# Optimization experiments

Measured on AMD Instinct MI355X. Metric: run time of the kernel, lower is better.

Reference implementation:

```python
import jax, jax.numpy as jnp
import numpy as np
from jax import lax

H = W = 8
N = H * W            # grid cells
D = 34               # token dim = 16 + 16 + 2
NH = 2               # attention heads
FF = 2048            # torch TransformerEncoderLayer default dim_feedforward
EPS = 1e-5


def setup_inputs():
    key = jax.random.key(0)
    ks = iter(jax.random.split(key, 64))
    rn = lambda shape, s=0.05: jax.random.normal(next(ks), shape, jnp.float32) * s
    inp = {"obs": jax.random.normal(next(ks), (2, H, W), jnp.float32), "action": 2}
    inp["conv1_w"] = rn((16, 2, 3, 3)); inp["conv1_b"] = rn((16,))
    inp["conv2_w"] = rn((16, 16, 3, 3)); inp["conv2_b"] = rn((16,))
    for l in range(2):
        p = f"l{l}_"
        inp[p + "in_w"] = rn((3 * D, D)); inp[p + "in_b"] = rn((3 * D,))
        inp[p + "out_w"] = rn((D, D)); inp[p + "out_b"] = rn((D,))
        inp[p + "ff1_w"] = rn((FF, D)); inp[p + "ff1_b"] = rn((FF,))
        inp[p + "ff2_w"] = rn((D, FF)); inp[p + "ff2_b"] = rn((D,))
        inp[p + "ln1_g"] = jnp.ones((D,)); inp[p + "ln1_b"] = jnp.zeros((D,))
        inp[p + "ln2_g"] = jnp.ones((D,)); inp[p + "ln2_b"] = jnp.zeros((D,))
    inp["act_w"] = rn((8, 4)); inp["act_b"] = rn((8,))
    inp["head_w"] = rn((16, D + 8)); inp["head_b"] = rn((16,))
    return inp


def _ln(x, g, b):
    m = x.mean(-1, keepdims=True)
    v = ((x - m) ** 2).mean(-1, keepdims=True)
    return (x - m) * lax.rsqrt(v + EPS) * g + b


def _mha(x, in_w, in_b, out_w, out_b):
    S = x.shape[0]
    hd = D // NH
    qkv = x @ in_w.T + in_b                          # [S, 3D]
    q, k, v = jnp.split(qkv, 3, axis=-1)
    q = q.reshape(S, NH, hd).transpose(1, 0, 2)      # [H, S, hd]
    k = k.reshape(S, NH, hd).transpose(1, 0, 2)
    v = v.reshape(S, NH, hd).transpose(1, 0, 2)
    attn = jax.nn.softmax(jnp.einsum('hsd,htd->hst', q, k) * (1.0 / float(np.sqrt(hd))), axis=-1)
    o = jnp.einsum('hst,htd->hsd', attn, v).transpose(1, 0, 2).reshape(S, D)
    return o @ out_w.T + out_b


def _layer(x, in_w, in_b, out_w, out_b, ff1_w, ff1_b, ff2_w, ff2_b, ln1_g, ln1_b, ln2_g, ln2_b):
    # torch default post-norm, relu activation, dropout off (eval)
    x = _ln(x + _mha(x, in_w, in_b, out_w, out_b), ln1_g, ln1_b)
    h = jax.nn.relu(x @ ff1_w.T + ff1_b) @ ff2_w.T + ff2_b
    return _ln(x + h, ln2_g, ln2_b)


def _forward(obs, conv1_w, conv1_b, conv2_w, conv2_b, layers, act_w, act_b, head_w, head_b, action):
    x = obs[None]                                    # [1, 2, H, W]
    dn = ('NCHW', 'OIHW', 'NCHW')
    x = jax.nn.relu(lax.conv_general_dilated(x, conv1_w, (1, 1), 'SAME', dimension_numbers=dn) + conv1_b[None, :, None, None])
    x = jax.nn.relu(lax.conv_general_dilated(x, conv2_w, (1, 1), 'SAME', dimension_numbers=dn) + conv2_b[None, :, None, None])
    cell = x.reshape(16, N).T                        # [N, 16]
    # vectorized pairwise relation tokens (replaces O(N^2) python loop)
    r = (jnp.arange(N) // W).astype(jnp.float32)
    c = (jnp.arange(N) % W).astype(jnp.float32)
    dx = (r[:, None] - r[None, :]) / ((H - 1) / 2.0)
    dy = (c[:, None] - c[None, :]) / ((W - 1) / 2.0)
    rel = jnp.stack([dx, dy], axis=-1)               # [N, N, 2]
    a = jnp.broadcast_to(cell[:, None, :], (N, N, 16))
    b = jnp.broadcast_to(cell[None, :, :], (N, N, 16))
    seq = jnp.concatenate([a, b, rel], axis=-1).reshape(N * N, D)
    for p in layers:
        seq = _layer(seq, *p)
    agent_idx = jnp.argmax(obs[0].reshape(-1))
    agent_tok = lax.dynamic_slice_in_dim(seq, agent_idx * N, N, 0)  # rows for agent cell
    hvec = agent_tok.mean(0)
    a_emb = jax.nn.relu(jax.nn.one_hot(action, 4, dtype=jnp.float32) @ act_w.T + act_b)
    return (jnp.concatenate([hvec, a_emb]) @ head_w.T + head_b)[None]


def reference(obs, action, conv1_w, conv1_b, conv2_w, conv2_b,
              l0_in_w, l0_in_b, l0_out_w, l0_out_b, l0_ff1_w, l0_ff1_b, l0_ff2_w, l0_ff2_b,
              l0_ln1_g, l0_ln1_b, l0_ln2_g, l0_ln2_b,
              l1_in_w, l1_in_b, l1_out_w, l1_out_b, l1_ff1_w, l1_ff1_b, l1_ff2_w, l1_ff2_b,
              l1_ln1_g, l1_ln1_b, l1_ln2_g, l1_ln2_b,
              act_w, act_b, head_w, head_b):
    layers = [
        (l0_in_w, l0_in_b, l0_out_w, l0_out_b, l0_ff1_w, l0_ff1_b, l0_ff2_w, l0_ff2_b, l0_ln1_g, l0_ln1_b, l0_ln2_g, l0_ln2_b),
        (l1_in_w, l1_in_b, l1_out_w, l1_out_b, l1_ff1_w, l1_ff1_b, l1_ff2_w, l1_ff2_b, l1_ln1_g, l1_ln1_b, l1_ln2_g, l1_ln2_b),
    ]
    return _forward(obs, conv1_w, conv1_b, conv2_w, conv2_b, layers, act_w, act_b, head_w, head_b, action)
```

## Files before the change

### kernel.cpp

```cpp
#include <hip/hip_runtime.h>
#include <math.h>

#define SEQ 4096
#define DIM 34
#define NHEAD 2
#define HD 17
#define FFDIM 2048
#define SC2 0.34990494f

#define EXP2F(x) __builtin_amdgcn_exp2f(x)
#define MFMA16(a, b, c) __builtin_amdgcn_mfma_f32_16x16x32_bf16(a, b, c, 0, 0, 0)

typedef unsigned short u16;
typedef __attribute__((ext_vector_type(8))) short bf16x8;
typedef __attribute__((ext_vector_type(4))) float f32x4;

__device__ inline u16 f2bf(float f) {
    uint32_t u = __builtin_bit_cast(uint32_t, f);
    u += 0x7fffu + ((u >> 16) & 1u);
    return (u16)(u >> 16);
}
__device__ inline uint32_t pack2(float a, float b) {
    uint32_t ua = __builtin_bit_cast(uint32_t, a);
    ua += 0x7fffu + ((ua >> 16) & 1u);
    uint32_t ub = __builtin_bit_cast(uint32_t, b);
    ub += 0x7fffu + ((ub >> 16) & 1u);
    return (ua >> 16) | (ub & 0xffff0000u);
}

#define W1B_ELEMS (FFDIM * 64)
#define W2B_ELEMS (48 * FFDIM)
#define NWCONV 448
#define NQT (SEQ / 16)

__global__ __launch_bounds__(1024) void wm_pre(
    const float* __restrict__ obs,
    const float* __restrict__ c1w, const float* __restrict__ c1b,
    const float* __restrict__ c2w, const float* __restrict__ c2b,
    const float* __restrict__ in_w, const float* __restrict__ in_b,
    float* __restrict__ x, u16* __restrict__ Qb, u16* __restrict__ Kb,
    u16* __restrict__ Vc, u16* __restrict__ V16)
{
    const int tid = threadIdx.x;
    __shared__ float obsp[2][10][10];
    __shared__ float h1p[16][10][10];
    __shared__ float cs[64][17];
    const int sb = blockIdx.x;
    const int t0 = sb * 64;

    for (int e = tid; e < 200; e += 1024) ((float*)obsp)[e] = 0.f;
    for (int e = tid; e < 1600; e += 1024) ((float*)h1p)[e] = 0.f;
    __syncthreads();
    if (tid < 128) {
        int i = tid >> 6, n = tid & 63, y = n >> 3, xx = n & 7;
        obsp[i][y + 1][xx + 1] = obs[tid];
    }
    __syncthreads();
    {
        int o = tid >> 6, n = tid & 63, y = n >> 3, xx = n & 7;
        float a = c1b[o];
        #pragma unroll
        for (int i = 0; i < 2; ++i)
            #pragma unroll
            for (int ky = 0; ky < 3; ++ky)
                #pragma unroll
                for (int kx = 0; kx < 3; ++kx)
                    a = fmaf(obsp[i][y + ky][xx + kx], c1w[((o*2 + i)*3 + ky)*3 + kx], a);
        h1p[o][y + 1][xx + 1] = fmaxf(a, 0.f);
    }
    __syncthreads();
    {
        int o = tid >> 6, n = tid & 63, y = n >> 3, xx = n & 7;
        float a = c2b[o];
        #pragma unroll
        for (int i = 0; i < 16; ++i)
            #pragma unroll
            for (int ky = 0; ky < 3; ++ky)
                #pragma unroll
                for (int kx = 0; kx < 3; ++kx)
                    a = fmaf(h1p[i][y + ky][xx + kx], c2w[((o*16 + i)*3 + ky)*3 + kx], a);
        cs[n][o] = fmaxf(a, 0.f);
    }
    __syncthreads();
    for (int e = tid; e < 64 * DIM; e += 1024) {
        int tl = e / DIM, d = e % DIM;
        int t = t0 + tl, i = t >> 6, j = t & 63;
        float v;
        if (d < 16)       v = cs[i][d];
        else if (d < 32)  v = cs[j][d - 16];
        else if (d == 32) v = (float)((i >> 3) - (j >> 3)) * (1.0f / 3.5f);
        else              v = (float)((i & 7) - (j & 7)) * (1.0f / 3.5f);
        x[t0 * DIM + e] = v;
    }
    for (int ii = 0; ii < 11; ++ii) {
        int e = tid + ii * 1024;
        if (e >= 64 * 162) break;
        int t = t0 + (e & 63), slot = e >> 6;
        int i = t >> 6, j = t & 63;
        float dx = (float)((i >> 3) - (j >> 3)) * (1.0f / 3.5f);
        float dy = (float)((i & 7) - (j & 7)) * (1.0f / 3.5f);
        if (slot < 128) {
            int isK = slot >> 6, h2 = (slot >> 5) & 1, hs = slot & 31;
            float val = 0.f;
            if (hs < HD) {
                int row = isK*DIM + h2*HD + hs;
                const float* wr = in_w + row*DIM;
                float a = in_b[row];
                #pragma unroll
                for (int d = 0; d < 16; ++d) a = fmaf(cs[i][d], wr[d], a);
                #pragma unroll
                for (int d = 0; d < 16; ++d) a = fmaf(cs[j][d], wr[16 + d], a);
                a = fmaf(dx, wr[32], a);
                a = fmaf(dy, wr[33], a);
                val = isK ? a : a * SC2;
            } else if (hs == HD) {
                val = isK ? 1.0f : -8.0f;
            }
            u16* dst = isK ? Kb : Qb;
            dst[(((size_t)h2*SEQ + t) << 5) + hs] = f2bf(val);
        } else {
            int s = slot - 128;
            int h2 = s >= HD, dd = s - h2*HD;
            int row = 2*DIM + h2*HD + dd;
            const float* wr = in_w + row*DIM;
            float a = in_b[row];
            #pragma unroll
            for (int d = 0; d < 16; ++d) a = fmaf(cs[i][d], wr[d], a);
            #pragma unroll
            for (int d = 0; d < 16; ++d) a = fmaf(cs[j][d], wr[16 + d], a);
            a = fmaf(dx, wr[32], a);
            a = fmaf(dy, wr[33], a);
            u16 v = f2bf(a);
            if (dd == 16) V16[h2*SEQ + t] = v;
            else {
                int c = t >> 5, g = (t >> 3) & 3, ix = t & 7;
                Vc[((((size_t)h2*128 + c)*4 + g)*16 + dd)*8 + ix] = v;
            }
        }
    }
}

__global__ __launch_bounds__(1024) void wm_attn3(const u16* __restrict__ Qb,
        const u16* __restrict__ Kb, const u16* __restrict__ Vc,
        const u16* __restrict__ V16, float* __restrict__ x,
        const float* __restrict__ ow, const float* __restrict__ obias,
        const float* __restrict__ g, const float* __restrict__ be,
        const float* __restrict__ w1a, const float* __restrict__ b1a, const float* __restrict__ w2a,
        const float* __restrict__ w1b, const float* __restrict__ b1b, const float* __restrict__ w2b,
        u16* __restrict__ W1A, u16* __restrict__ W2A,
        u16* __restrict__ W1B, u16* __restrict__ W2B)
{
    const int qt = blockIdx.x;
    const int tid = threadIdx.x;
    if (qt >= NQT) {
        int id = (qt - NQT) * 1024 + tid;
        const int half = W1B_ELEMS + W2B_ELEMS;
        const float* w1 = w1a; const float* b1 = b1a; const float* w2 = w2a;
        u16* W1 = W1A; u16* W2 = W2A;
        if (id >= half) { id -= half; w1 = w1b; b1 = b1b; w2 = w2b; W1 = W1B; W2 = W2B; }
        if (id < W1B_ELEMS) {
            int n = id >> 6, c = id & 63;
            float v = (c < DIM) ? w1[n*DIM + c] : ((c == DIM) ? b1[n] : 0.f);
            W1[id] = f2bf(v);
        } else {
            int e = id - W1B_ELEMS;
            int n = e >> 11;
            float v = (n < DIM) ? w2[(n << 11) + (e & 2047)] : 0.f;
            W2[e] = f2bf(v);
        }
        return;
    }
    const int wv = tid >> 6, l = tid & 63;
    const int h = wv >> 3, rr = wv & 7;
    const int q = l & 15, gg = l >> 4;

    __shared__ float red[16][64][7];
    __shared__ float os[16][DIM];
    __shared__ float ys[16][DIM];
    __shared__ float stats[16][2];

    const u16* Qh = Qb + (((size_t)h*SEQ + qt*16 + q) << 5) + 8*gg;
    const u16* Kh = Kb + ((size_t)h*SEQ << 5);
    const u16* Vh = Vc + (size_t)h*128*512;
    const u16* V6 = V16 + (size_t)h*SEQ;

    const bf16x8 qf = *(const bf16x8*)Qh;
    const f32x4 zero4 = {0.f, 0.f, 0.f, 0.f};
    bf16x8 onesv;
    { union { uint32_t u[4]; bf16x8 v; } o1;
      o1.u[0] = o1.u[1] = o1.u[2] = o1.u[3] = 0x3F803F80u; onesv = o1.v; }

    f32x4 olo = zero4, ohi = zero4;
    const int srcA = q + 32*(gg & 1);
    const int srcB = srcA + 16;
    const bool hi = (gg >= 2);

    for (int it = 0; it < 8; ++it) {
        const int cA = rr*16 + it*2;
        const int k0 = cA * 32;
        bf16x8 kf0 = *(const bf16x8*)(Kh + ((size_t)(k0 + q) << 5) + 8*gg);
        bf16x8 kf1 = *(const bf16x8*)(Kh + ((size_t)(k0 + 16 + q) << 5) + 8*gg);
        bf16x8 kf2 = *(const bf16x8*)(Kh + ((size_t)(k0 + 32 + q) << 5) + 8*gg);
        bf16x8 kf3 = *(const bf16x8*)(Kh + ((size_t)(k0 + 48 + q) << 5) + 8*gg);
        f32x4 s0 = MFMA16(kf0, qf, zero4);
        f32x4 s1 = MFMA16(kf1, qf, zero4);
        f32x4 s2 = MFMA16(kf2, qf, zero4);
        f32x4 s3 = MFMA16(kf3, qf, zero4);
        float pa0 = EXP2F(s0[0]), pa1 = EXP2F(s0[1]), pa2 = EXP2F(s0[2]), pa3 = EXP2F(s0[3]);
        float pa4 = EXP2F(s1[0]), pa5 = EXP2F(s1[1]), pa6 = EXP2F(s1[2]), pa7 = EXP2F(s1[3]);
        float pb0 = EXP2F(s2[0]), pb1 = EXP2F(s2[1]), pb2 = EXP2F(s2[2]), pb3 = EXP2F(s2[3]);
        float pb4 = EXP2F(s3[0]), pb5 = EXP2F(s3[1]), pb6 = EXP2F(s3[2]), pb7 = EXP2F(s3[3]);
        {
            uint32_t a0t0 = pack2(pa0, pa1), a1t0 = pack2(pa2, pa3);
            uint32_t a0t1 = pack2(pa4, pa5), a1t1 = pack2(pa6, pa7);
            uint32_t w0a = (uint32_t)__shfl((int)a0t0, srcA), w0b = (uint32_t)__shfl((int)a0t1, srcA);
            uint32_t w1a_ = (uint32_t)__shfl((int)a1t0, srcA), w1b_ = (uint32_t)__shfl((int)a1t1, srcA);
            uint32_t w2a_ = (uint32_t)__shfl((int)a0t0, srcB), w2b_ = (uint32_t)__shfl((int)a0t1, srcB);
            uint32_t w3a = (uint32_t)__shfl((int)a1t0, srcB), w3b = (uint32_t)__shfl((int)a1t1, srcB);
            union { uint32_t u[4]; bf16x8 v; } pu;
            pu.u[0] = hi ? w0b : w0a;
            pu.u[1] = hi ? w1b_ : w1a_;
            pu.u[2] = hi ? w2b_ : w2a_;
            pu.u[3] = hi ? w3b : w3a;
            bf16x8 vf = *(const bf16x8*)(Vh + (size_t)(cA*4 + gg)*128 + q*8);
            bf16x8 v6 = {};
            if (q == 0) v6 = *(const bf16x8*)(V6 + k0 + 8*gg);
            else if (q == 1) v6 = onesv;
            olo = MFMA16(vf, pu.v, olo);
            ohi = MFMA16(v6, pu.v, ohi);
        }
        {
            uint32_t a0t0 = pack2(pb0, pb1), a1t0 = pack2(pb2, pb3);
            uint32_t a0t1 = pack2(pb4, pb5), a1t1 = pack2(pb6, pb7);
            uint32_t w0a = (uint32_t)__shfl((int)a0t0, srcA), w0b = (uint32_t)__shfl((int)a0t1, srcA);
            uint32_t w1a_ = (uint32_t)__shfl((int)a1t0, srcA), w1b_ = (uint32_t)__shfl((int)a1t1, srcA);
            uint32_t w2a_ = (uint32_t)__shfl((int)a0t0, srcB), w2b_ = (uint32_t)__shfl((int)a0t1, srcB);
            uint32_t w3a = (uint32_t)__shfl((int)a1t0, srcB), w3b = (uint32_t)__shfl((int)a1t1, srcB);
            union { uint32_t u[4]; bf16x8 v; } pu;
            pu.u[0] = hi ? w0b : w0a;
            pu.u[1] = hi ? w1b_ : w1a_;
            pu.u[2] = hi ? w2b_ : w2a_;
            pu.u[3] = hi ? w3b : w3a;
            bf16x8 vf = *(const bf16x8*)(Vh + (size_t)((cA + 1)*4 + gg)*128 + q*8);
            bf16x8 v6 = {};
            if (q == 0) v6 = *(const bf16x8*)(V6 + k0 + 32 + 8*gg);
            else if (q == 1) v6 = onesv;
            olo = MFMA16(vf, pu.v, olo);
            ohi = MFMA16(v6, pu.v, ohi);
        }
    }

    {
        float* r = red[wv][l];
        r[0] = ohi[1];
        r[1] = olo[0]; r[2] = olo[1]; r[3] = olo[2]; r[4] = olo[3];
        r[5] = ohi[0];
    }
    __syncthreads();
    if (rr == 0) {
        float lt = 0.f, o0 = 0.f, o1 = 0.f, o2 = 0.f, o3 = 0.f, o6 = 0.f;
        #pragma unroll
        for (int p = 0; p < 8; ++p) {
            float* r = red[wv + p][l];
            lt += r[0]; o0 += r[1]; o1 += r[2]; o2 += r[3]; o3 += r[4]; o6 += r[5];
        }
        lt += __shfl_xor(lt, 16);
        lt += __shfl_xor(lt, 32);
        float inv = 1.f / lt;
        os[q][h*HD + 4*gg + 0] = o0*inv;
        os[q][h*HD + 4*gg + 1] = o1*inv;
        os[q][h*HD + 4*gg + 2] = o2*inv;
        os[q][h*HD + 4*gg + 3] = o3*inv;
        if (gg == 0) os[q][h*HD + 16] = o6*inv;
    }
    __syncthreads();
    for (int e = tid; e < 16 * DIM; e += 1024) {
        int tt = e / DIM, d = e % DIM;
        const float* wr = ow + d*DIM;
        float acc = obias[d];
        #pragma unroll
        for (int k = 0; k < DIM; ++k) acc = fmaf(os[tt][k], wr[k], acc);
        ys[tt][d] = x[(size_t)(qt*16 + tt)*DIM + d] + acc;
    }
    __syncthreads();
    if (tid < 16) {
        float s1 = 0.f, s2 = 0.f;
        #pragma unroll
        for (int d = 0; d < DIM; ++d) { float v = ys[tid][d]; s1 += v; s2 += v*v; }
        float mean = s1 * (1.0f / DIM);
        float var  = s2 * (1.0f / DIM) - mean*mean;
        stats[tid][0] = mean;
        stats[tid][1] = rsqrtf(var + 1e-5f);
    }
    __syncthreads();
    for (int e = tid; e < 16 * DIM; e += 1024) {
        int tt = e / DIM, d = e % DIM;
        x[(size_t)(qt*16 + tt)*DIM + d] = (ys[tt][d] - stats[tt][0]) * stats[tt][1] * g[d] + be[d];
    }
}

__global__ __launch_bounds__(1024) void wm_ff3(float* __restrict__ x,
        const u16* __restrict__ W1b, const u16* __restrict__ W2b,
        const float* __restrict__ b2, const float* __restrict__ g,
        const float* __restrict__ be,
        const float* __restrict__ in_w, const float* __restrict__ in_b,
        u16* __restrict__ Qb, u16* __restrict__ Kb,
        u16* __restrict__ Vc, u16* __restrict__ V16, int do_qkv)
{
    __shared__ u16 Hs[16][16][128];
    __shared__ float red[16][16][52];
    __shared__ float ys[16][DIM];
    __shared__ float stats[16][2];
    const int tid = threadIdx.x, wv = tid >> 6, l = tid & 63;
    const int q = l & 15, g4 = l >> 4;
    const int t0 = blockIdx.x * 16;

    const float* xr = x + (size_t)(t0 + q) * DIM;
    union { uint32_t u[4]; bf16x8 v; } a0, a1;
    #pragma unroll
    for (int j = 0; j < 4; ++j)
        a0.u[j] = pack2(xr[g4*8 + 2*j], xr[g4*8 + 2*j + 1]);
    a1.u[0] = 0; a1.u[1] = 0; a1.u[2] = 0; a1.u[3] = 0;
    if (g4 == 0) {
        a1.u[0] = pack2(xr[32], xr[33]);
        a1.u[1] = pack2(1.0f, 0.f);
    }
    const f32x4 zero4 = {0.f, 0.f, 0.f, 0.f};

    const int hbase = wv * 128;
    #pragma unroll
    for (int nt = 0; nt < 8; ++nt) {
        const u16* brow = W1b + (size_t)(hbase + nt*16 + q) * 64 + g4*8;
        bf16x8 b0 = *(const bf16x8*)brow;
        bf16x8 b1f = *(const bf16x8*)(brow + 32);
        f32x4 c = MFMA16(a0.v, b0, zero4);
        c = MFMA16(a1.v, b1f, c);
        #pragma unroll
        for (int r = 0; r < 4; ++r) {
            int mm = 4*g4 + r;
            int byte = ((nt*16 + q) * 2) ^ ((mm & 7) << 4);
            *(u16*)((char*)&Hs[wv][mm][0] + byte) = f2bf(fmaxf(c[r], 0.f));
        }
    }
    asm volatile("s_waitcnt lgkmcnt(0)" ::: "memory");
    __builtin_amdgcn_sched_barrier(0);
    f32x4 acc0 = zero4, acc1 = zero4, acc2 = zero4;
    #pragma unroll
    for (int ks = 0; ks < 4; ++ks) {
        int byte = (ks*64 + g4*16) ^ ((q & 7) << 4);
        bf16x8 af = *(const bf16x8*)((char*)&Hs[wv][q][0] + byte);
        const u16* bp = W2b + (size_t)q * FFDIM + hbase + ks*32 + g4*8;
        acc0 = MFMA16(af, *(const bf16x8*)bp, acc0);
        acc1 = MFMA16(af, *(const bf16x8*)(bp + 16*FFDIM), acc1);
        acc2 = MFMA16(af, *(const bf16x8*)(bp + 32*FFDIM), acc2);
    }
    #pragma unroll
    for (int r = 0; r < 4; ++r) {
        red[wv][4*g4 + r][q]      = acc0[r];
        red[wv][4*g4 + r][16 + q] = acc1[r];
        red[wv][4*g4 + r][32 + q] = acc2[r];
    }
    __syncthreads();
    for (int e = tid; e < 16*DIM; e += 1024) {
        int tt = e / DIM, d = e % DIM;
        float v = x[(size_t)(t0 + tt)*DIM + d] + b2[d];
        #pragma unroll
        for (int w = 0; w < 16; ++w) v += red[w][tt][d];
        ys[tt][d] = v;
    }
    __syncthreads();
    if (tid < 16) {
        float s1 = 0.f, s2 = 0.f;
        #pragma unroll
        for (int d = 0; d < DIM; ++d) { float v = ys[tid][d]; s1 += v; s2 += v * v; }
        float mean = s1 * (1.0f / DIM);
        float var  = s2 * (1.0f / DIM) - mean * mean;
        stats[tid][0] = mean;
        stats[tid][1] = rsqrtf(var + 1e-5f);
    }
    __syncthreads();
    for (int e = tid; e < 16*DIM; e += 1024) {
        int tt = e / DIM, d = e % DIM;
        float v = (ys[tt][d] - stats[tt][0]) * stats[tt][1] * g[d] + be[d];
        x[(size_t)(t0 + tt)*DIM + d] = v;
        ys[tt][d] = v;
    }
    if (do_qkv) {
        __syncthreads();
        #pragma unroll
        for (int ii = 0; ii < 2; ++ii) {
            int e = tid + ii*1024;
            if (e < 16*102) {
                int r = e >> 4, tt = e & 15;
                const float* wr = in_w + r*DIM;
                float a = in_b[r];
                #pragma unroll
                for (int d = 0; d < DIM; ++d) a = fmaf(ys[tt][d], wr[d], a);
                int tg = t0 + tt;
                if (r < 68) {
                    int rq = (r < 34) ? r : r - 34;
                    int h2 = rq >= HD, hs = rq - h2*HD;
                    u16 v = f2bf((r < 34) ? a*SC2 : a);
                    u16* dst = (r < 34) ? Qb : Kb;
                    dst[(((size_t)h2*SEQ + tg) << 5) + hs] = v;
                } else {
                    int rv = r - 68;
                    int h2 = rv >= HD, dd = rv - h2*HD;
                    u16 v = f2bf(a);
                    if (dd == 16) V16[h2*SEQ + tg] = v;
                    else {
                        int c = tg >> 5, gg = (tg >> 3) & 3, ix = tg & 7;
                        Vc[((((size_t)h2*128 + c)*4 + gg)*16 + dd)*8 + ix] = v;
                    }
                }
            }
        }
    }
}

__global__ __launch_bounds__(64) void wm_final(const float* __restrict__ x,
        const float* __restrict__ obs, const int* __restrict__ action,
        const float* __restrict__ aw, const float* __restrict__ ab,
        const float* __restrict__ hw, const float* __restrict__ hb,
        float* __restrict__ out)
{
    __shared__ float hv[DIM];
    __shared__ float saemb[8];
    __shared__ int sai;
    const int tid = threadIdx.x;
    {
        float v = obs[tid];
        float mx = v;
        for (int off = 32; off; off >>= 1) mx = fmaxf(mx, __shfl_xor(mx, off));
        unsigned long long mask = __ballot(v == mx);
        if (tid == 0) sai = (int)(__ffsll(mask) - 1);
    }
    if (tid < 8) {
        int act = *action;
        saemb[tid] = fmaxf(aw[tid*4 + act] + ab[tid], 0.f);
    }
    __syncthreads();
    const int ai = sai;
    if (tid < DIM) {
        float s = 0.f;
        for (int r = 0; r < 64; ++r) s += x[(size_t)(ai*64 + r)*DIM + tid];
        hv[tid] = s * (1.0f / 64.0f);
    }
    __syncthreads();
    if (tid < 16) {
        float a = hb[tid];
        #pragma unroll
        for (int d = 0; d < DIM; ++d) a = fmaf(hv[d], hw[tid*42 + d], a);
        #pragma unroll
        for (int j = 0; j < 8; ++j) a = fmaf(saemb[j], hw[tid*42 + DIM + j], a);
        out[tid] = a;
    }
}

extern "C" void kernel_launch(void* const* d_in, const int* in_sizes, int n_in,
                              void* d_out, int out_size, void* d_ws, size_t ws_size,
                              hipStream_t stream)
{
    const float* obs    = (const float*)d_in[0];
    const int*   action = (const int*)  d_in[1];

    float* ws   = (float*)d_ws;
    float* x    = ws + 1056;
    float* o    = x + SEQ * DIM;
    u16*   Qb   = (u16*)(o + SEQ * DIM);
    u16*   Kb   = Qb + 2 * SEQ * 32;
    u16*   Vc   = Kb + 2 * SEQ * 32;
    u16*   V16  = Vc + 2 * 128 * 512;
    u16*   W1b0 = V16 + 2 * SEQ;
    u16*   W2b0 = W1b0 + W1B_ELEMS;
    u16*   W1b1 = W2b0 + W2B_ELEMS;
    u16*   W2b1 = W1b1 + W1B_ELEMS;

    wm_pre<<<64, 1024, 0, stream>>>(
        obs, (const float*)d_in[2], (const float*)d_in[3],
        (const float*)d_in[4], (const float*)d_in[5],
        (const float*)d_in[6], (const float*)d_in[7],
        x, Qb, Kb, Vc, V16);

    wm_attn3<<<NQT + NWCONV, 1024, 0, stream>>>(Qb, Kb, Vc, V16, x,
        (const float*)d_in[8], (const float*)d_in[9],
        (const float*)d_in[14], (const float*)d_in[15],
        (const float*)d_in[10], (const float*)d_in[11], (const float*)d_in[12],
        (const float*)d_in[22], (const float*)d_in[23], (const float*)d_in[24],
        W1b0, W2b0, W1b1, W2b1);

    wm_ff3<<<NQT, 1024, 0, stream>>>(x, W1b0, W2b0,
        (const float*)d_in[13], (const float*)d_in[16], (const float*)d_in[17],
        (const float*)d_in[18], (const float*)d_in[19],
        Qb, Kb, Vc, V16, 1);

    wm_attn3<<<NQT, 1024, 0, stream>>>(Qb, Kb, Vc, V16, x,
        (const float*)d_in[20], (const float*)d_in[21],
        (const float*)d_in[26], (const float*)d_in[27],
        (const float*)d_in[10], (const float*)d_in[11], (const float*)d_in[12],
        (const float*)d_in[22], (const float*)d_in[23], (const float*)d_in[24],
        W1b0, W2b0, W1b1, W2b1);

    wm_ff3<<<NQT, 1024, 0, stream>>>(x, W1b1, W2b1,
        (const float*)d_in[25], (const float*)d_in[28], (const float*)d_in[29],
        (const float*)d_in[18], (const float*)d_in[19],
        Qb, Kb, Vc, V16, 0);

    wm_final<<<1, 64, 0, stream>>>(x, obs, action,
        (const float*)d_in[30], (const float*)d_in[31],
        (const float*)d_in[32], (const float*)d_in[33], (float*)d_out);
}
```

Before: 95.93 us.

## Split attention keys across two blocks and fuse out-proj/LN1 into FF kernel

Each query tile's attention is now split into two blocks, each covering half the keys. Each block writes unnormalized partial outputs and softmax denominators to a workspace buffer. The FF kernel combines the two partials, normalizes, and then applies the output projection and LN1 before the feed-forward step. This doubles attention-grid parallelism and removes the serial epilogue from the attention kernel, at the cost of extra global traffic for the partials and more work in the FF kernel.

After: 96.16 us. Within noise of the previous version (+0.2%).

```diff
diff --git a/kernel.cpp b/kernel.cpp
--- a/kernel.cpp
+++ b/kernel.cpp
@@ -32,6 +32,7 @@
 #define W2B_ELEMS (48 * FFDIM)
 #define NWCONV 448
 #define NQT (SEQ / 16)
+#define POS 36
 
 __global__ __launch_bounds__(1024) void wm_pre(
     const float* __restrict__ obs,
@@ -140,20 +141,18 @@
     }
 }
 
-__global__ __launch_bounds__(1024) void wm_attn3(const u16* __restrict__ Qb,
+__global__ __launch_bounds__(1024, 8) void wm_attn5(const u16* __restrict__ Qb,
         const u16* __restrict__ Kb, const u16* __restrict__ Vc,
-        const u16* __restrict__ V16, float* __restrict__ x,
-        const float* __restrict__ ow, const float* __restrict__ obias,
-        const float* __restrict__ g, const float* __restrict__ be,
+        const u16* __restrict__ V16, float* __restrict__ po,
         const float* __restrict__ w1a, const float* __restrict__ b1a, const float* __restrict__ w2a,
         const float* __restrict__ w1b, const float* __restrict__ b1b, const float* __restrict__ w2b,
         u16* __restrict__ W1A, u16* __restrict__ W2A,
         u16* __restrict__ W1B, u16* __restrict__ W2B)
 {
-    const int qt = blockIdx.x;
+    const int bid = blockIdx.x;
     const int tid = threadIdx.x;
-    if (qt >= NQT) {
-        int id = (qt - NQT) * 1024 + tid;
+    if (bid >= 2 * NQT) {
+        int id = (bid - 2 * NQT) * 1024 + tid;
         const int half = W1B_ELEMS + W2B_ELEMS;
         const float* w1 = w1a; const float* b1 = b1a; const float* w2 = w2a;
         u16* W1 = W1A; u16* W2 = W2A;
@@ -170,14 +169,12 @@
         }
         return;
     }
+    const int qt = bid >> 1, khalf = bid & 1;
     const int wv = tid >> 6, l = tid & 63;
     const int h = wv >> 3, rr = wv & 7;
     const int q = l & 15, gg = l >> 4;
 
     __shared__ float red[16][64][7];
-    __shared__ float os[16][DIM];
-    __shared__ float ys[16][DIM];
-    __shared__ float stats[16][2];
 
     const u16* Qh = Qb + (((size_t)h*SEQ + qt*16 + q) << 5) + 8*gg;
     const u16* Kh = Kb + ((size_t)h*SEQ << 5);
@@ -195,8 +192,8 @@
     const int srcB = srcA + 16;
     const bool hi = (gg >= 2);
 
-    for (int it = 0; it < 8; ++it) {
-        const int cA = rr*16 + it*2;
+    for (int it = 0; it < 4; ++it) {
+        const int cA = khalf*64 + rr*8 + it*2;
         const int k0 = cA * 32;
         bf16x8 kf0 = *(const bf16x8*)(Kh + ((size_t)(k0 + q) << 5) + 8*gg);
         bf16x8 kf1 = *(const bf16x8*)(Kh + ((size_t)(k0 + 16 + q) << 5) + 8*gg);
@@ -266,40 +263,19 @@
         }
         lt += __shfl_xor(lt, 16);
         lt += __shfl_xor(lt, 32);
-        float inv = 1.f / lt;
-        os[q][h*HD + 4*gg + 0] = o0*inv;
-        os[q][h*HD + 4*gg + 1] = o1*inv;
-        os[q][h*HD + 4*gg + 2] = o2*inv;
-        os[q][h*HD + 4*gg + 3] = o3*inv;
-        if (gg == 0) os[q][h*HD + 16] = o6*inv;
-    }
-    __syncthreads();
-    for (int e = tid; e < 16 * DIM; e += 1024) {
-        int tt = e / DIM, d = e % DIM;
-        const float* wr = ow + d*DIM;
-        float acc = obias[d];
-        #pragma unroll
-        for (int k = 0; k < DIM; ++k) acc = fmaf(os[tt][k], wr[k], acc);
-        ys[tt][d] = x[(size_t)(qt*16 + tt)*DIM + d] + acc;
-    }
-    __syncthreads();
-    if (tid < 16) {
-        float s1 = 0.f, s2 = 0.f;
-        #pragma unroll
-        for (int d = 0; d < DIM; ++d) { float v = ys[tid][d]; s1 += v; s2 += v*v; }
-        float mean = s1 * (1.0f / DIM);
-        float var  = s2 * (1.0f / DIM) - mean*mean;
-        stats[tid][0] = mean;
-        stats[tid][1] = rsqrtf(var + 1e-5f);
-    }
-    __syncthreads();
-    for (int e = tid; e < 16 * DIM; e += 1024) {
-        int tt = e / DIM, d = e % DIM;
-        x[(size_t)(qt*16 + tt)*DIM + d] = (ys[tt][d] - stats[tt][0]) * stats[tt][1] * g[d] + be[d];
+        float* prow = po + ((size_t)khalf*SEQ + qt*16 + q) * POS;
+        prow[h*HD + 4*gg + 0] = o0;
+        prow[h*HD + 4*gg + 1] = o1;
+        prow[h*HD + 4*gg + 2] = o2;
+        prow[h*HD + 4*gg + 3] = o3;
+        if (gg == 0) { prow[h*HD + 16] = o6; prow[34 + h] = lt; }
     }
 }
 
 __global__ __launch_bounds__(1024) void wm_ff3(float* __restrict__ x,
+        const float* __restrict__ po,
+        const float* __restrict__ ow, const float* __restrict__ obias,
+        const float* __restrict__ ln1g, const float* __restrict__ ln1b,
         const u16* __restrict__ W1b, const u16* __restrict__ W2b,
         const float* __restrict__ b2, const float* __restrict__ g,
         const float* __restrict__ be,
@@ -307,22 +283,60 @@
         u16* __restrict__ Qb, u16* __restrict__ Kb,
         u16* __restrict__ Vc, u16* __restrict__ V16, int do_qkv)
 {
-    __shared__ u16 Hs[16][16][128];
+    __shared__ union { u16 Hs[16][16][128]; float os[16][POS]; } sa;
     __shared__ float red[16][16][52];
     __shared__ float ys[16][DIM];
     __shared__ float stats[16][2];
+    __shared__ float xt[16][DIM + 2];
     const int tid = threadIdx.x, wv = tid >> 6, l = tid & 63;
     const int q = l & 15, g4 = l >> 4;
     const int t0 = blockIdx.x * 16;
 
-    const float* xr = x + (size_t)(t0 + q) * DIM;
+    for (int e = tid; e < 16 * POS; e += 1024) {
+        int tt = e / POS, c = e % POS;
+        sa.os[tt][c] = po[(size_t)(t0 + tt)*POS + c]
+                     + po[(size_t)(SEQ + t0 + tt)*POS + c];
+    }
+    __syncthreads();
+    if (tid < 32) stats[tid >> 1][tid & 1] = 1.f / sa.os[tid >> 1][34 + (tid & 1)];
+    __syncthreads();
+    for (int e = tid; e < 16 * DIM; e += 1024) {
+        int tt = e / DIM, d = e % DIM;
+        sa.os[tt][d] *= stats[tt][d >= HD];
+    }
+    __syncthreads();
+    for (int e = tid; e < 16 * DIM; e += 1024) {
+        int tt = e / DIM, d = e % DIM;
+        const float* wr = ow + d*DIM;
+        float acc = obias[d];
+        #pragma unroll
+        for (int k = 0; k < DIM; ++k) acc = fmaf(sa.os[tt][k], wr[k], acc);
+        ys[tt][d] = x[(size_t)(t0 + tt)*DIM + d] + acc;
+    }
+    __syncthreads();
+    if (tid < 16) {
+        float s1 = 0.f, s2 = 0.f;
+        #pragma unroll
+        for (int d = 0; d < DIM; ++d) { float v = ys[tid][d]; s1 += v; s2 += v*v; }
+        float mean = s1 * (1.0f / DIM);
+        float var  = s2 * (1.0f / DIM) - mean*mean;
+        stats[tid][0] = mean;
+        stats[tid][1] = rsqrtf(var + 1e-5f);
+    }
+    __syncthreads();
+    for (int e = tid; e < 16 * DIM; e += 1024) {
+        int tt = e / DIM, d = e % DIM;
+        xt[tt][d] = (ys[tt][d] - stats[tt][0]) * stats[tt][1] * ln1g[d] + ln1b[d];
+    }
+    __syncthreads();
+
     union { uint32_t u[4]; bf16x8 v; } a0, a1;
     #pragma unroll
     for (int j = 0; j < 4; ++j)
-        a0.u[j] = pack2(xr[g4*8 + 2*j], xr[g4*8 + 2*j + 1]);
+        a0.u[j] = pack2(xt[q][g4*8 + 2*j], xt[q][g4*8 + 2*j + 1]);
     a1.u[0] = 0; a1.u[1] = 0; a1.u[2] = 0; a1.u[3] = 0;
     if (g4 == 0) {
-        a1.u[0] = pack2(xr[32], xr[33]);
+        a1.u[0] = pack2(xt[q][32], xt[q][33]);
         a1.u[1] = pack2(1.0f, 0.f);
     }
     const f32x4 zero4 = {0.f, 0.f, 0.f, 0.f};
@@ -339,7 +353,7 @@
         for (int r = 0; r < 4; ++r) {
             int mm = 4*g4 + r;
             int byte = ((nt*16 + q) * 2) ^ ((mm & 7) << 4);
-            *(u16*)((char*)&Hs[wv][mm][0] + byte) = f2bf(fmaxf(c[r], 0.f));
+            *(u16*)((char*)&sa.Hs[wv][mm][0] + byte) = f2bf(fmaxf(c[r], 0.f));
         }
     }
     asm volatile("s_waitcnt lgkmcnt(0)" ::: "memory");
@@ -348,7 +362,7 @@
     #pragma unroll
     for (int ks = 0; ks < 4; ++ks) {
         int byte = (ks*64 + g4*16) ^ ((q & 7) << 4);
-        bf16x8 af = *(const bf16x8*)((char*)&Hs[wv][q][0] + byte);
+        bf16x8 af = *(const bf16x8*)((char*)&sa.Hs[wv][q][0] + byte);
         const u16* bp = W2b + (size_t)q * FFDIM + hbase + ks*32 + g4*8;
         acc0 = MFMA16(af, *(const bf16x8*)bp, acc0);
         acc1 = MFMA16(af, *(const bf16x8*)(bp + 16*FFDIM), acc1);
@@ -363,7 +377,7 @@
     __syncthreads();
     for (int e = tid; e < 16*DIM; e += 1024) {
         int tt = e / DIM, d = e % DIM;
-        float v = x[(size_t)(t0 + tt)*DIM + d] + b2[d];
+        float v = xt[tt][d] + b2[d];
         #pragma unroll
         for (int w = 0; w < 16; ++w) v += red[w][tt][d];
         ys[tt][d] = v;
@@ -475,6 +489,7 @@
     u16*   W2b0 = W1b0 + W1B_ELEMS;
     u16*   W1b1 = W2b0 + W2B_ELEMS;
     u16*   W2b1 = W1b1 + W1B_ELEMS;
+    float* po   = (float*)(W2b1 + W2B_ELEMS);
 
     wm_pre<<<64, 1024, 0, stream>>>(
         obs, (const float*)d_in[2], (const float*)d_in[3],
@@ -482,26 +497,28 @@
         (const float*)d_in[6], (const float*)d_in[7],
         x, Qb, Kb, Vc, V16);
 
-    wm_attn3<<<NQT + NWCONV, 1024, 0, stream>>>(Qb, Kb, Vc, V16, x,
-        (const float*)d_in[8], (const float*)d_in[9],
-        (const float*)d_in[14], (const float*)d_in[15],
+    wm_attn5<<<2*NQT + NWCONV, 1024, 0, stream>>>(Qb, Kb, Vc, V16, po,
         (const float*)d_in[10], (const float*)d_in[11], (const float*)d_in[12],
         (const float*)d_in[22], (const float*)d_in[23], (const float*)d_in[24],
         W1b0, W2b0, W1b1, W2b1);
 
-    wm_ff3<<<NQT, 1024, 0, stream>>>(x, W1b0, W2b0,
+    wm_ff3<<<NQT, 1024, 0, stream>>>(x, po,
+        (const float*)d_in[8], (const float*)d_in[9],
+        (const float*)d_in[14], (const float*)d_in[15],
+        W1b0, W2b0,
         (const float*)d_in[13], (const float*)d_in[16], (const float*)d_in[17],
         (const float*)d_in[18], (const float*)d_in[19],
         Qb, Kb, Vc, V16, 1);
 
-    wm_attn3<<<NQT, 1024, 0, stream>>>(Qb, Kb, Vc, V16, x,
-        (const float*)d_in[20], (const float*)d_in[21],
-        (const float*)d_in[26], (const float*)d_in[27],
+    wm_attn5<<<2*NQT, 1024, 0, stream>>>(Qb, Kb, Vc, V16, po,
         (const float*)d_in[10], (const float*)d_in[11], (const float*)d_in[12],
         (const float*)d_in[22], (const float*)d_in[23], (const float*)d_in[24],
         W1b0, W2b0, W1b1, W2b1);
 
-    wm_ff3<<<NQT, 1024, 0, stream>>>(x, W1b1, W2b1,
+    wm_ff3<<<NQT, 1024, 0, stream>>>(x, po,
+        (const float*)d_in[20], (const float*)d_in[21],
+        (const float*)d_in[26], (const float*)d_in[27],
+        W1b1, W2b1,
         (const float*)d_in[25], (const float*)d_in[28], (const float*)d_in[29],
         (const float*)d_in[18], (const float*)d_in[19],
         Qb, Kb, Vc, V16, 0);
```

## Halve rows per FF block and split prologue into more blocks

Applied to the files above, without the earlier changes.

The feed-forward kernel now handles 8 tokens per block instead of 16, launching twice as many blocks. MFMA tiles are still 16 rows, so half of each tile is zero-padded, and the LDS buffers and swizzle are resized to match. The pre kernel also spreads its token and QKV work over 256 blocks of 16 tokens instead of 64 blocks of 64. The aim is better CU occupancy and load spread across the GPU. The cost is MFMA work wasted on padded rows and the per-block weight reads (W1/W2) being repeated twice as often, and the pre kernel now recomputes the convolution in four times as many blocks.

Result: slower. 113.3 us (+18.1%).

```diff
diff --git a/kernel.cpp b/kernel.cpp
--- a/kernel.cpp
+++ b/kernel.cpp
@@ -45,8 +45,7 @@
     __shared__ float obsp[2][10][10];
     __shared__ float h1p[16][10][10];
     __shared__ float cs[64][17];
-    const int sb = blockIdx.x;
-    const int t0 = sb * 64;
+    const int t0 = blockIdx.x * 16;
 
     for (int e = tid; e < 200; e += 1024) ((float*)obsp)[e] = 0.f;
     for (int e = tid; e < 1600; e += 1024) ((float*)h1p)[e] = 0.f;
@@ -82,7 +81,7 @@
         cs[n][o] = fmaxf(a, 0.f);
     }
     __syncthreads();
-    for (int e = tid; e < 64 * DIM; e += 1024) {
+    for (int e = tid; e < 16 * DIM; e += 1024) {
         int tl = e / DIM, d = e % DIM;
         int t = t0 + tl, i = t >> 6, j = t & 63;
         float v;
@@ -90,12 +89,12 @@
         else if (d < 32)  v = cs[j][d - 16];
         else if (d == 32) v = (float)((i >> 3) - (j >> 3)) * (1.0f / 3.5f);
         else              v = (float)((i & 7) - (j & 7)) * (1.0f / 3.5f);
-        x[t0 * DIM + e] = v;
-    }
-    for (int ii = 0; ii < 11; ++ii) {
+        x[(size_t)t0 * DIM + e] = v;
+    }
+    for (int ii = 0; ii < 3; ++ii) {
         int e = tid + ii * 1024;
-        if (e >= 64 * 162) break;
-        int t = t0 + (e & 63), slot = e >> 6;
+        if (e >= 16 * 162) break;
+        int t = t0 + (e & 15), slot = e >> 4;
         int i = t >> 6, j = t & 63;
         float dx = (float)((i >> 3) - (j >> 3)) * (1.0f / 3.5f);
         float dy = (float)((i & 7) - (j & 7)) * (1.0f / 3.5f);
@@ -299,7 +298,7 @@
     }
 }
 
-__global__ __launch_bounds__(1024) void wm_ff3(float* __restrict__ x,
+__global__ __launch_bounds__(1024, 8) void wm_ff3(float* __restrict__ x,
         const u16* __restrict__ W1b, const u16* __restrict__ W2b,
         const float* __restrict__ b2, const float* __restrict__ g,
         const float* __restrict__ be,
@@ -307,23 +306,26 @@
         u16* __restrict__ Qb, u16* __restrict__ Kb,
         u16* __restrict__ Vc, u16* __restrict__ V16, int do_qkv)
 {
-    __shared__ u16 Hs[16][16][128];
-    __shared__ float red[16][16][52];
-    __shared__ float ys[16][DIM];
-    __shared__ float stats[16][2];
+    __shared__ u16 Hs[16][8][128];
+    __shared__ float red[16][8][52];
+    __shared__ float ys[8][DIM];
+    __shared__ float stats[8][2];
     const int tid = threadIdx.x, wv = tid >> 6, l = tid & 63;
     const int q = l & 15, g4 = l >> 4;
-    const int t0 = blockIdx.x * 16;
-
-    const float* xr = x + (size_t)(t0 + q) * DIM;
+    const int t0 = blockIdx.x * 8;
+
     union { uint32_t u[4]; bf16x8 v; } a0, a1;
-    #pragma unroll
-    for (int j = 0; j < 4; ++j)
-        a0.u[j] = pack2(xr[g4*8 + 2*j], xr[g4*8 + 2*j + 1]);
+    a0.u[0] = 0; a0.u[1] = 0; a0.u[2] = 0; a0.u[3] = 0;
     a1.u[0] = 0; a1.u[1] = 0; a1.u[2] = 0; a1.u[3] = 0;
-    if (g4 == 0) {
-        a1.u[0] = pack2(xr[32], xr[33]);
-        a1.u[1] = pack2(1.0f, 0.f);
+    if (q < 8) {
+        const float* xr = x + (size_t)(t0 + q) * DIM;
+        #pragma unroll
+        for (int j = 0; j < 4; ++j)
+            a0.u[j] = pack2(xr[g4*8 + 2*j], xr[g4*8 + 2*j + 1]);
+        if (g4 == 0) {
+            a1.u[0] = pack2(xr[32], xr[33]);
+            a1.u[1] = pack2(1.0f, 0.f);
+        }
     }
     const f32x4 zero4 = {0.f, 0.f, 0.f, 0.f};
 
@@ -335,11 +337,13 @@
         bf16x8 b1f = *(const bf16x8*)(brow + 32);
         f32x4 c = MFMA16(a0.v, b0, zero4);
         c = MFMA16(a1.v, b1f, c);
-        #pragma unroll
-        for (int r = 0; r < 4; ++r) {
-            int mm = 4*g4 + r;
-            int byte = ((nt*16 + q) * 2) ^ ((mm & 7) << 4);
-            *(u16*)((char*)&Hs[wv][mm][0] + byte) = f2bf(fmaxf(c[r], 0.f));
+        if (g4 < 2) {
+            #pragma unroll
+            for (int r = 0; r < 4; ++r) {
+                int mm = 4*g4 + r;
+                int byte = ((nt*16 + q) * 2) ^ (mm << 5);
+                *(u16*)((char*)&Hs[wv][mm][0] + byte) = f2bf(fmaxf(c[r], 0.f));
+            }
         }
     }
     asm volatile("s_waitcnt lgkmcnt(0)" ::: "memory");
@@ -347,21 +351,26 @@
     f32x4 acc0 = zero4, acc1 = zero4, acc2 = zero4;
     #pragma unroll
     for (int ks = 0; ks < 4; ++ks) {
-        int byte = (ks*64 + g4*16) ^ ((q & 7) << 4);
-        bf16x8 af = *(const bf16x8*)((char*)&Hs[wv][q][0] + byte);
+        bf16x8 af = {};
+        if (q < 8) {
+            int byte = (ks*64 + g4*16) ^ (q << 5);
+            af = *(const bf16x8*)((char*)&Hs[wv][q][0] + byte);
+        }
         const u16* bp = W2b + (size_t)q * FFDIM + hbase + ks*32 + g4*8;
         acc0 = MFMA16(af, *(const bf16x8*)bp, acc0);
         acc1 = MFMA16(af, *(const bf16x8*)(bp + 16*FFDIM), acc1);
         acc2 = MFMA16(af, *(const bf16x8*)(bp + 32*FFDIM), acc2);
     }
-    #pragma unroll
-    for (int r = 0; r < 4; ++r) {
-        red[wv][4*g4 + r][q]      = acc0[r];
-        red[wv][4*g4 + r][16 + q] = acc1[r];
-        red[wv][4*g4 + r][32 + q] = acc2[r];
-    }
-    __syncthreads();
-    for (int e = tid; e < 16*DIM; e += 1024) {
+    if (g4 < 2) {
+        #pragma unroll
+        for (int r = 0; r < 4; ++r) {
+            red[wv][4*g4 + r][q]      = acc0[r];
+            red[wv][4*g4 + r][16 + q] = acc1[r];
+            red[wv][4*g4 + r][32 + q] = acc2[r];
+        }
+    }
+    __syncthreads();
+    for (int e = tid; e < 8*DIM; e += 1024) {
         int tt = e / DIM, d = e % DIM;
         float v = x[(size_t)(t0 + tt)*DIM + d] + b2[d];
         #pragma unroll
@@ -369,7 +378,7 @@
         ys[tt][d] = v;
     }
     __syncthreads();
-    if (tid < 16) {
+    if (tid < 8) {
         float s1 = 0.f, s2 = 0.f;
         #pragma unroll
         for (int d = 0; d < DIM; ++d) { float v = ys[tid][d]; s1 += v; s2 += v * v; }
@@ -379,7 +388,7 @@
         stats[tid][1] = rsqrtf(var + 1e-5f);
     }
     __syncthreads();
-    for (int e = tid; e < 16*DIM; e += 1024) {
+    for (int e = tid; e < 8*DIM; e += 1024) {
         int tt = e / DIM, d = e % DIM;
         float v = (ys[tt][d] - stats[tt][0]) * stats[tt][1] * g[d] + be[d];
         x[(size_t)(t0 + tt)*DIM + d] = v;
@@ -387,11 +396,10 @@
     }
     if (do_qkv) {
         __syncthreads();
-        #pragma unroll
-        for (int ii = 0; ii < 2; ++ii) {
-            int e = tid + ii*1024;
-            if (e < 16*102) {
-                int r = e >> 4, tt = e & 15;
+        {
+            int e = tid;
+            if (e < 8*102) {
+                int r = e >> 3, tt = e & 7;
                 const float* wr = in_w + r*DIM;
                 float a = in_b[r];
                 #pragma unroll
@@ -476,7 +484,7 @@
     u16*   W1b1 = W2b0 + W2B_ELEMS;
     u16*   W2b1 = W1b1 + W1B_ELEMS;
 
-    wm_pre<<<64, 1024, 0, stream>>>(
+    wm_pre<<<256, 1024, 0, stream>>>(
         obs, (const float*)d_in[2], (const float*)d_in[3],
         (const float*)d_in[4], (const float*)d_in[5],
         (const float*)d_in[6], (const float*)d_in[7],
@@ -489,7 +497,7 @@
         (const float*)d_in[22], (const float*)d_in[23], (const float*)d_in[24],
         W1b0, W2b0, W1b1, W2b1);
 
-    wm_ff3<<<NQT, 1024, 0, stream>>>(x, W1b0, W2b0,
+    wm_ff3<<<SEQ / 8, 1024, 0, stream>>>(x, W1b0, W2b0,
         (const float*)d_in[13], (const float*)d_in[16], (const float*)d_in[17],
         (const float*)d_in[18], (const float*)d_in[19],
         Qb, Kb, Vc, V16, 1);
@@ -501,7 +509,7 @@
         (const float*)d_in[22], (const float*)d_in[23], (const float*)d_in[24],
         W1b0, W2b0, W1b1, W2b1);
 
-    wm_ff3<<<NQT, 1024, 0, stream>>>(x, W1b1, W2b1,
+    wm_ff3<<<SEQ / 8, 1024, 0, stream>>>(x, W1b1, W2b1,
         (const float*)d_in[25], (const float*)d_in[28], (const float*)d_in[29],
         (const float*)d_in[18], (const float*)d_in[19],
         Qb, Kb, Vc, V16, 0);
```
